# Performance work log

Measured on AMD Instinct MI355X. Metric: run time of the kernel, lower is better.

The kernel has to match this reference:

```python
import jax, jax.numpy as jnp
import numpy as np

H = 48; W = 48; WS = 8; NH = 12; FTH = 0.4; EPS = 1e-6


def _layernorm(x, w, b):
    mu = jnp.mean(x, axis=-1, keepdims=True)
    var = jnp.mean((x - mu) ** 2, axis=-1, keepdims=True)
    return (x - mu) * jax.lax.rsqrt(var + EPS) * w + b


def _mha(x, w_qkv, b_qkv, w_o, b_o, key_mask=None):
    # x: (Bn, N, C); w_qkv: (3, C, C); key_mask: (Bn, N) bool or None
    Bn, N, C = x.shape
    d = C // NH
    qkv = jnp.einsum('bnc,tcd->tbnd', x, w_qkv) + b_qkv[:, None, None, :]
    q, k, v = [t.reshape(Bn, N, NH, d).transpose(0, 2, 1, 3) for t in qkv]
    s = jnp.einsum('bhqd,bhkd->bhqk', q, k) / jnp.sqrt(jnp.asarray(d, x.dtype))
    if key_mask is not None:
        s = jnp.where(key_mask[:, None, None, :], s, jnp.asarray(-1e9, s.dtype))
    p = jax.nn.softmax(s, axis=-1)
    ctx = jnp.einsum('bhqk,bhkd->bhqd', p, v).transpose(0, 2, 1, 3).reshape(Bn, N, C)
    return ctx @ w_o + b_o


def _forward(x, mask, w_qkv_g, b_qkv_g, w_o_g, b_o_g, w_qkv_l, b_qkv_l, w_o_l, b_o_l,
             ln1_w, ln1_b, ln2_w, ln2_b, w_fc1, b_fc1, w_fc2, b_fc2):
    B, L, C = x.shape
    shortcut = x
    xn = _layernorm(x, ln1_w, ln1_b)

    # avg_pool2d(mask, 4, 4) -> (B, H, W); fg/bg split
    pooled = mask.reshape(B, 1, H, 4, W, 4).mean(axis=(3, 5))[:, 0]      # (B,H,W)
    fg = pooled > FTH                                                    # bool (B,H,W)
    fg_tok = fg.reshape(B, L)
    bg = (~fg).astype(x.dtype)
    # window-level bg mask: avg_pool(bg, WS) > 0 -> window contains any bg token
    bg_win = bg.reshape(B, H // WS, WS, W // WS, WS).mean(axis=(2, 4)) > 0.0   # (B, nH, nW)
    bg_win_tok = jnp.broadcast_to(bg_win[:, :, None, :, None],
                                  (B, H // WS, WS, W // WS, WS)).reshape(B, L)

    # local windowed attention on all windows (equivalent on bg windows; masked out elsewhere)
    xw = xn.reshape(B, H // WS, WS, W // WS, WS, C).transpose(0, 1, 3, 2, 4, 5)
    xw = xw.reshape(-1, WS * WS, C)                                      # (B*nWin, WS*WS, C)
    lout = _mha(xw, w_qkv_l, b_qkv_l, w_o_l, b_o_l)
    lout = lout.reshape(B, H // WS, W // WS, WS, WS, C).transpose(0, 1, 3, 2, 4, 5)
    lout = lout.reshape(B, L, C)

    # global attention with fg key mask (fg queries attend fg keys only)
    gout = _mha(xn, w_qkv_g, b_qkv_g, w_o_g, b_o_g, key_mask=fg_tok)

    # scatter-back semantics: fg positions take global output; bg-window positions take local output; rest zero
    zero = jnp.zeros((), x.dtype)
    x_new = jnp.where(fg_tok[..., None], gout,
                      jnp.where(bg_win_tok[..., None], lout, zero))

    x1 = shortcut + x_new
    h = _layernorm(x1, ln2_w, ln2_b)
    h = jax.nn.gelu(h @ w_fc1 + b_fc1, approximate=False) @ w_fc2 + b_fc2
    return x1 + h


def setup_inputs() -> dict:
    key = jax.random.key(0)
    ks = jax.random.split(key, 8)
    B, L, C, M = 2, H * W, 768, 3072
    s = 0.02
    return {
        'x': jax.random.normal(ks[0], (B, L, C), jnp.float32),
        'mask': jax.random.uniform(ks[1], (B, 1, 4 * H, 4 * W), jnp.float32),
        'w_qkv_g': jax.random.normal(ks[2], (3, C, C), jnp.float32) * s,
        'b_qkv_g': jnp.zeros((3, C), jnp.float32),
        'w_o_g': jax.random.normal(ks[3], (C, C), jnp.float32) * s,
        'b_o_g': jnp.zeros((C,), jnp.float32),
        'w_qkv_l': jax.random.normal(ks[4], (3, C, C), jnp.float32) * s,
        'b_qkv_l': jnp.zeros((3, C), jnp.float32),
        'w_o_l': jax.random.normal(ks[5], (C, C), jnp.float32) * s,
        'b_o_l': jnp.zeros((C,), jnp.float32),
        'ln1_w': jnp.ones((C,), jnp.float32),
        'ln1_b': jnp.zeros((C,), jnp.float32),
        'ln2_w': jnp.ones((C,), jnp.float32),
        'ln2_b': jnp.zeros((C,), jnp.float32),
        'w_fc1': jax.random.normal(ks[6], (C, M), jnp.float32) * s,
        'b_fc1': jnp.zeros((M,), jnp.float32),
        'w_fc2': jax.random.normal(ks[7], (M, C), jnp.float32) * s,
        'b_fc2': jnp.zeros((C,), jnp.float32),
    }


def reference(x, mask, w_qkv_g, b_qkv_g, w_o_g, b_o_g, w_qkv_l, b_qkv_l, w_o_l, b_o_l,
              ln1_w, ln1_b, ln2_w, ln2_b, w_fc1, b_fc1, w_fc2, b_fc2):
    return _forward(x, mask, w_qkv_g, b_qkv_g, w_o_g, b_o_g, w_qkv_l, b_qkv_l, w_o_l, b_o_l,
                    ln1_w, ln1_b, ln2_w, ln2_b, w_fc1, b_fc1, w_fc2, b_fc2)
```

## Files before the change

### kernel.cpp

```cpp
#include <hip/hip_runtime.h>
#include <math.h>

#define Lh 2304
#define Ch 768
#define NHh 12
#define Bh 2
#define QS2 3072

typedef unsigned short ushort_t;
typedef unsigned int uint_t;
typedef __attribute__((ext_vector_type(8))) short bf16x8;
typedef __attribute__((ext_vector_type(4))) float f32x4;
#define MFMA16(a, b, c) __builtin_amdgcn_mfma_f32_16x16x32_bf16(a, b, c, 0, 0, 0)

#define SCL2 0.18033688f
#define MSK2 1.4426950e9f
#if __has_builtin(__builtin_amdgcn_exp2f)
#define EXP2F(x) __builtin_amdgcn_exp2f(x)
#else
#define EXP2F(x) exp2f(x)
#endif

__device__ __forceinline__ ushort_t f2bf(float f) {
    union { float f; uint_t u; } v; v.f = f;
    uint_t u = v.u + 0x7fffu + ((v.u >> 16) & 1u);
    return (ushort_t)(u >> 16);
}
__device__ __forceinline__ uint_t pack2bf(float a, float b) {
    return (uint_t)f2bf(a) | ((uint_t)f2bf(b) << 16);
}

__device__ __forceinline__ void llds16(ushort_t* dst, const ushort_t* src) {
    __builtin_amdgcn_global_load_lds(
        (__attribute__((address_space(1))) void*)(const_cast<ushort_t*>(src)),
        (__attribute__((address_space(3))) void*)dst, 16, 0, 0);
}

__global__ __launch_bounds__(256)
void layernorm_bf16_kernel(const float* __restrict__ x, const float* __restrict__ w,
                           const float* __restrict__ b, ushort_t* __restrict__ y)
{
    int row = blockIdx.x;
    int tid = threadIdx.x;
    const float* xr = x + (size_t)row * Ch;
    float v0 = xr[tid], v1 = xr[tid + 256], v2 = xr[tid + 512];
    __shared__ float red[256];
    red[tid] = v0 + v1 + v2;
    __syncthreads();
    for (int st = 128; st > 0; st >>= 1) {
        if (tid < st) red[tid] += red[tid + st];
        __syncthreads();
    }
    float mean = red[0] * (1.0f / 768.0f);
    __syncthreads();
    float d0 = v0 - mean, d1 = v1 - mean, d2 = v2 - mean;
    red[tid] = d0 * d0 + d1 * d1 + d2 * d2;
    __syncthreads();
    for (int st = 128; st > 0; st >>= 1) {
        if (tid < st) red[tid] += red[tid + st];
        __syncthreads();
    }
    float rstd = rsqrtf(red[0] * (1.0f / 768.0f) + 1e-6f);
    ushort_t* yr = y + (size_t)row * Ch;
    yr[tid]       = f2bf(d0 * rstd * w[tid]       + b[tid]);
    yr[tid + 256] = f2bf(d1 * rstd * w[tid + 256] + b[tid + 256]);
    yr[tid + 512] = f2bf(d2 * rstd * w[tid + 512] + b[tid + 512]);
}

__global__ __launch_bounds__(64)
void mask_kernel(const float* __restrict__ mask, float* __restrict__ fg,
                 float* __restrict__ bgw)
{
    int win = blockIdx.x;
    int b = win / 36, w = win % 36;
    int wi = w / 6, wj = w % 6;
    int lane = threadIdx.x;
    int i = wi * 8 + (lane >> 3), j = wj * 8 + (lane & 7);
    const float* mb = mask + (size_t)b * 192 * 192 + (size_t)(i * 4) * 192 + j * 4;
    float s = 0.0f;
    #pragma unroll
    for (int di = 0; di < 4; ++di) {
        float4 v = *(const float4*)(mb + (size_t)di * 192);
        s += v.x + v.y + v.z + v.w;
    }
    float f = (s * (1.0f / 16.0f) > 0.4f) ? 1.0f : 0.0f;
    fg[b * Lh + i * 48 + j] = f;
    unsigned long long bg = __ballot(f == 0.0f);
    if (lane == 0) bgw[win] = bg ? 1.0f : 0.0f;
}

__global__ __launch_bounds__(256)
void transpose_all_kernel(const float* __restrict__ w_qkv_g, const float* __restrict__ w_qkv_l,
                          const float* __restrict__ w_o_g, const float* __restrict__ w_o_l,
                          const float* __restrict__ w_fc1, const float* __restrict__ w_fc2,
                          ushort_t* __restrict__ wtq, ushort_t* __restrict__ wt_o_g,
                          ushort_t* __restrict__ wt_o_l, ushort_t* __restrict__ wt_fc1,
                          ushort_t* __restrict__ wt_fc2)
{
    int blk = blockIdx.x;
    const float* W; ushort_t* D; int K, N, nx, bx;
    const size_t CC = (size_t)Ch * Ch;
    if (blk < 432)       { int t = blk / 144; bx = blk % 144;
                           W = w_qkv_g + t * CC; D = wtq + t * CC; K = 768; N = 768; nx = 12; }
    else if (blk < 864)  { int r = blk - 432; int t = r / 144; bx = r % 144;
                           W = w_qkv_l + t * CC; D = wtq + (size_t)2304 * 768 + t * CC;
                           K = 768; N = 768; nx = 12; }
    else if (blk < 1008) { bx = blk - 864;  W = w_o_g; D = wt_o_g; K = 768; N = 768; nx = 12; }
    else if (blk < 1152) { bx = blk - 1008; W = w_o_l; D = wt_o_l; K = 768; N = 768; nx = 12; }
    else if (blk < 1728) { bx = blk - 1152; W = w_fc1; D = wt_fc1; K = 768; N = 3072; nx = 48; }
    else                 { bx = blk - 1728; W = w_fc2; D = wt_fc2; K = 3072; N = 768; nx = 12; }
    int n0 = (bx % nx) * 64;
    int k0 = (bx / nx) * 64;
    int tid = threadIdx.x;
    __shared__ float T[64][65];
    #pragma unroll
    for (int i = 0; i < 16; ++i) {
        int lin = i * 256 + tid;
        int r = lin >> 6, c = lin & 63;
        T[r][c] = W[(size_t)(k0 + r) * N + n0 + c];
    }
    __syncthreads();
    #pragma unroll
    for (int i = 0; i < 4; ++i) {
        int lin = i * 256 + tid;
        int r = lin >> 4, c0 = (lin & 15) * 4;
        uint_t lo = pack2bf(T[c0][r], T[c0 + 1][r]);
        uint_t hi = pack2bf(T[c0 + 2][r], T[c0 + 3][r]);
        *(uint2*)&D[(size_t)(n0 + r) * K + k0 + c0] = make_uint2(lo, hi);
    }
}

template<int BNt, int VMODE>
__global__ __launch_bounds__(256)
void gemm_bf16_t(const ushort_t* __restrict__ A, const ushort_t* __restrict__ Bt,
                 const float* __restrict__ bias, const float* __restrict__ residual,
                 void* __restrict__ C, ushort_t* __restrict__ vt,
                 int M, int N, int K, int flags)
{
    __shared__ ushort_t AsL[2][128 * 32];
    __shared__ ushort_t BsL[2][BNt * 32];
    int bm = blockIdx.y * 128;
    int bx = blockIdx.x;
    int bn;
    if (VMODE == 1) {
        bn = (bx < 6) ? 1536 + bx * 128 : 3840 + (bx - 6) * 128;
    } else if (flags & 4) {
        bn = (bx < 12) ? bx * 128 : 2304 + (bx - 12) * 128;
    } else {
        bn = bx * BNt;
    }
    int tid = threadIdx.x;
    int lane = tid & 63;
    int wave = tid >> 6;
    int wm = wave >> 1, wn = wave & 1;
    int quad = lane >> 4, l15 = lane & 15;
    constexpr int NJ = BNt / 32;

    int srow = lane >> 2;
    int sg8 = ((lane & 3) ^ ((lane >> 3) & 3)) * 8;
    int fsw = (l15 >> 1) & 3;

    f32x4 acc[4][NJ];
    #pragma unroll
    for (int i = 0; i < 4; ++i)
        #pragma unroll
        for (int j = 0; j < NJ; ++j)
            acc[i][j] = (f32x4){0.f, 0.f, 0.f, 0.f};

    int iters = K / 32;
    llds16(&AsL[0][wave * 512], A + (size_t)(bm + wave * 16 + srow) * K + sg8);
    llds16(&AsL[0][(wave + 4) * 512], A + (size_t)(bm + (wave + 4) * 16 + srow) * K + sg8);
    llds16(&BsL[0][wave * 512], Bt + (size_t)(bn + wave * 16 + srow) * K + sg8);
    if (BNt == 128)
        llds16(&BsL[0][(wave + 4) * 512], Bt + (size_t)(bn + (wave + 4) * 16 + srow) * K + sg8);

    for (int kt = 0; kt < iters; ++kt) {
        int cur = kt & 1;
        __syncthreads();

        bf16x8 af[4], bfr[NJ];
        #pragma unroll
        for (int i = 0; i < 4; ++i)
            af[i] = *(const bf16x8*)&AsL[cur][(wm * 64 + i * 16 + l15) * 32 + ((quad ^ fsw) * 8)];
        #pragma unroll
        for (int j = 0; j < NJ; ++j)
            bfr[j] = *(const bf16x8*)&BsL[cur][(wn * (BNt / 2) + j * 16 + l15) * 32 + ((quad ^ fsw) * 8)];

        if (kt + 1 < iters) {
            int k0 = (kt + 1) * 32;
            int nxt = 1 - cur;
            llds16(&AsL[nxt][wave * 512], A + (size_t)(bm + wave * 16 + srow) * K + k0 + sg8);
            llds16(&AsL[nxt][(wave + 4) * 512], A + (size_t)(bm + (wave + 4) * 16 + srow) * K + k0 + sg8);
            llds16(&BsL[nxt][wave * 512], Bt + (size_t)(bn + wave * 16 + srow) * K + k0 + sg8);
            if (BNt == 128)
                llds16(&BsL[nxt][(wave + 4) * 512], Bt + (size_t)(bn + (wave + 4) * 16 + srow) * K + k0 + sg8);
        }

        if constexpr (VMODE == 0) {
            #pragma unroll
            for (int i = 0; i < 4; ++i)
                #pragma unroll
                for (int j = 0; j < NJ; ++j)
                    acc[i][j] = MFMA16(bfr[j], af[i], acc[i][j]);
        } else {
            #pragma unroll
            for (int i = 0; i < 4; ++i)
                #pragma unroll
                for (int j = 0; j < NJ; ++j)
                    acc[i][j] = MFMA16(af[i], bfr[j], acc[i][j]);
        }
    }

    if constexpr (VMODE == 1) {
        #pragma unroll
        for (int j = 0; j < NJ; ++j) {
            int col = bn + wn * (BNt / 2) + j * 16 + l15;
            int colp = col - ((col >= 3840) ? 3072 : 1536);
            float bc = bias[col];
            #pragma unroll
            for (int i = 0; i < 4; ++i) {
                int row0 = bm + wm * 64 + i * 16 + quad * 4;
                *(uint2*)&vt[(size_t)colp * 4608 + row0] =
                    make_uint2(pack2bf(acc[i][j][0] + bc, acc[i][j][1] + bc),
                               pack2bf(acc[i][j][2] + bc, acc[i][j][3] + bc));
            }
        }
        return;
    }

    #pragma unroll
    for (int i = 0; i < 4; ++i) {
        int row = bm + wm * 64 + i * 16 + l15;
        #pragma unroll
        for (int j = 0; j < NJ; ++j) {
            int col = bn + wn * (BNt / 2) + j * 16 + quad * 4;
            float4 bia = *(const float4*)&bias[col];
            float o0 = acc[i][j][0] + bia.x;
            float o1 = acc[i][j][1] + bia.y;
            float o2 = acc[i][j][2] + bia.z;
            float o3 = acc[i][j][3] + bia.w;
            if (flags & 1) {
                o0 = o0 * 0.5f * (1.0f + erff(o0 * 0.70710678f));
                o1 = o1 * 0.5f * (1.0f + erff(o1 * 0.70710678f));
                o2 = o2 * 0.5f * (1.0f + erff(o2 * 0.70710678f));
                o3 = o3 * 0.5f * (1.0f + erff(o3 * 0.70710678f));
            }
            if (residual) {
                float4 rs = *(const float4*)&residual[(size_t)row * N + col];
                o0 += rs.x; o1 += rs.y; o2 += rs.z; o3 += rs.w;
            }
            if (flags & 4) {
                int cq = col - ((col >= 2304) ? 768 : 0);
                *(uint2*)&((ushort_t*)C)[(size_t)row * QS2 + cq] =
                    make_uint2(pack2bf(o0, o1), pack2bf(o2, o3));
            } else if (flags & 2) {
                *(uint2*)&((ushort_t*)C)[(size_t)row * N + col] =
                    make_uint2(pack2bf(o0, o1), pack2bf(o2, o3));
            } else {
                *(float4*)&((float*)C)[(size_t)row * N + col] =
                    make_float4(o0, o1, o2, o3);
            }
        }
    }
}

__global__ __launch_bounds__(256)
void oproj_dual_kernel(const ushort_t* __restrict__ ctxg, const ushort_t* __restrict__ ctxl,
                       const ushort_t* __restrict__ Wg, const ushort_t* __restrict__ Wl,
                       const float* __restrict__ biasg, const float* __restrict__ biasl,
                       const float* __restrict__ x, float* __restrict__ x1,
                       const float* __restrict__ fg, const float* __restrict__ bgw)
{
    __shared__ ushort_t AsL[2][128 * 32];
    __shared__ ushort_t BsL[2][64 * 32];
    int bm = blockIdx.y * 128;
    int bn = blockIdx.x * 64;
    int tid = threadIdx.x;
    int lane = tid & 63;
    int wave = tid >> 6;
    int wm = wave >> 1, wn = wave & 1;
    int quad = lane >> 4, l15 = lane & 15;

    int srow = lane >> 2;
    int sg8 = ((lane & 3) ^ ((lane >> 3) & 3)) * 8;
    int fsw = (l15 >> 1) & 3;
    const int K = Ch, N = Ch, iters = Ch / 32;

    f32x4 accg[4][2], accl[4][2];
    #pragma unroll
    for (int i = 0; i < 4; ++i)
        #pragma unroll
        for (int j = 0; j < 2; ++j) {
            accg[i][j] = (f32x4){0.f, 0.f, 0.f, 0.f};
            accl[i][j] = (f32x4){0.f, 0.f, 0.f, 0.f};
        }

    #pragma unroll
    for (int pass = 0; pass < 2; ++pass) {
        const ushort_t* A = pass ? ctxl : ctxg;
        const ushort_t* Bt = pass ? Wl : Wg;
        if (pass) __syncthreads();
        llds16(&AsL[0][wave * 512], A + (size_t)(bm + wave * 16 + srow) * K + sg8);
        llds16(&AsL[0][(wave + 4) * 512], A + (size_t)(bm + (wave + 4) * 16 + srow) * K + sg8);
        llds16(&BsL[0][wave * 512], Bt + (size_t)(bn + wave * 16 + srow) * K + sg8);

        for (int kt = 0; kt < iters; ++kt) {
            int cur = kt & 1;
            __syncthreads();
            bf16x8 af[4], bfr[2];
            #pragma unroll
            for (int i = 0; i < 4; ++i)
                af[i] = *(const bf16x8*)&AsL[cur][(wm * 64 + i * 16 + l15) * 32 + ((quad ^ fsw) * 8)];
            #pragma unroll
            for (int j = 0; j < 2; ++j)
                bfr[j] = *(const bf16x8*)&BsL[cur][(wn * 32 + j * 16 + l15) * 32 + ((quad ^ fsw) * 8)];
            if (kt + 1 < iters) {
                int k0 = (kt + 1) * 32;
                int nxt = 1 - cur;
                llds16(&AsL[nxt][wave * 512], A + (size_t)(bm + wave * 16 + srow) * K + k0 + sg8);
                llds16(&AsL[nxt][(wave + 4) * 512], A + (size_t)(bm + (wave + 4) * 16 + srow) * K + k0 + sg8);
                llds16(&BsL[nxt][wave * 512], Bt + (size_t)(bn + wave * 16 + srow) * K + k0 + sg8);
            }
            if (pass == 0) {
                #pragma unroll
                for (int i = 0; i < 4; ++i)
                    #pragma unroll
                    for (int j = 0; j < 2; ++j)
                        accg[i][j] = MFMA16(bfr[j], af[i], accg[i][j]);
            } else {
                #pragma unroll
                for (int i = 0; i < 4; ++i)
                    #pragma unroll
                    for (int j = 0; j < 2; ++j)
                        accl[i][j] = MFMA16(bfr[j], af[i], accl[i][j]);
            }
        }
    }

    #pragma unroll
    for (int i = 0; i < 4; ++i) {
        int row = bm + wm * 64 + i * 16 + l15;
        int bb = (row >= Lh) ? 1 : 0;
        int n = row - bb * Lh;
        int ii = n / 48, jj = n % 48;
        float keepg = (fg[row] != 0.0f) ? 1.0f : 0.0f;
        float keepl = (keepg == 0.0f &&
                       bgw[bb * 36 + (ii >> 3) * 6 + (jj >> 3)] != 0.0f) ? 1.0f : 0.0f;
        #pragma unroll
        for (int j = 0; j < 2; ++j) {
            int col = bn + wn * 32 + j * 16 + quad * 4;
            float4 bg4 = *(const float4*)&biasg[col];
            float4 bl4 = *(const float4*)&biasl[col];
            float4 x4 = *(const float4*)&x[(size_t)row * N + col];
            float4 o;
            o.x = x4.x + keepg * (accg[i][j][0] + bg4.x) + keepl * (accl[i][j][0] + bl4.x);
            o.y = x4.y + keepg * (accg[i][j][1] + bg4.y) + keepl * (accl[i][j][1] + bl4.y);
            o.z = x4.z + keepg * (accg[i][j][2] + bg4.z) + keepl * (accl[i][j][2] + bl4.z);
            o.w = x4.w + keepg * (accg[i][j][3] + bg4.w) + keepl * (accl[i][j][3] + bl4.w);
            *(float4*)&x1[(size_t)row * N + col] = o;
        }
    }
}

__device__ __forceinline__ void attn_global_body(
    const ushort_t* __restrict__ QKV, const ushort_t* __restrict__ VT,
    const float* __restrict__ fg,
    float* __restrict__ Opart, float* __restrict__ Lpart,
    int tile, int h, int b, int half,
    ushort_t (*Ks)[2][64][32], ushort_t (*Vs)[2][64][32],
    ushort_t (*Ps)[72], float (*fgs)[64])
{
    int tid = threadIdx.x;
    int lane = tid & 63;
    int wave = tid >> 6;
    int quad = lane >> 4, l15 = lane & 15;
    int kb0 = half * 1152;

    bf16x8 aq[2][2];
    #pragma unroll
    for (int s = 0; s < 2; ++s) {
        int tok = tile * 128 + wave * 32 + s * 16 + l15;
        const ushort_t* qbase = QKV + (size_t)(b * Lh + tok) * QS2 + h * 64;
        #pragma unroll
        for (int step = 0; step < 2; ++step)
            aq[s][step] = *(const bf16x8*)(qbase + step * 32 + quad * 8);
    }

    int srow = lane >> 2;
    int sc = lane & 3;
    int krow = wave * 16 + srow;
    int scx = (sc ^ ((krow >> 1) & 3)) * 8;
    const ushort_t* ksrc = QKV + (size_t)(b * Lh + kb0 + krow) * QS2 + 768 + h * 64 + scx;
    const ushort_t* vsrc = VT + (size_t)(h * 64 + krow) * 4608 + b * Lh + kb0 + scx;

    float l_part[2] = {0.f, 0.f};
    f32x4 o_acc[2][4];
    #pragma unroll
    for (int s = 0; s < 2; ++s)
        #pragma unroll
        for (int t4 = 0; t4 < 4; ++t4) o_acc[s][t4] = (f32x4){0.f, 0.f, 0.f, 0.f};

    llds16(&Ks[0][0][wave * 16][0], ksrc);
    llds16(&Ks[0][1][wave * 16][0], ksrc + 32);
    llds16(&Vs[0][0][wave * 16][0], vsrc);
    llds16(&Vs[0][1][wave * 16][0], vsrc + 32);
    if (tid < 64) fgs[0][tid] = (fg[b * Lh + kb0 + tid] - 1.0f) * MSK2;

    int rfs = (l15 >> 1) & 3;

    for (int kt = 0; kt < 18; ++kt) {
        int cur = kt & 1, nxt = cur ^ 1;
        __syncthreads();

        bf16x8 bk[2][4];
        #pragma unroll
        for (int step = 0; step < 2; ++step)
            #pragma unroll
            for (int j4 = 0; j4 < 4; ++j4)
                bk[step][j4] = *(const bf16x8*)&Ks[cur][step][j4 * 16 + l15][(quad ^ rfs) * 8];

        if (kt + 1 < 18) {
            const ushort_t* kp = ksrc + (size_t)(kt + 1) * 64 * QS2;
            const ushort_t* vp = vsrc + (kt + 1) * 64;
            llds16(&Ks[nxt][0][wave * 16][0], kp);
            llds16(&Ks[nxt][1][wave * 16][0], kp + 32);
            llds16(&Vs[nxt][0][wave * 16][0], vp);
            llds16(&Vs[nxt][1][wave * 16][0], vp + 32);
            if (tid < 64) fgs[nxt][tid] = (fg[b * Lh + kb0 + (kt + 1) * 64 + tid] - 1.0f) * MSK2;
        }

        f32x4 s4[2][4];
        #pragma unroll
        for (int s = 0; s < 2; ++s)
            #pragma unroll
            for (int j4 = 0; j4 < 4; ++j4) s4[s][j4] = (f32x4){0.f, 0.f, 0.f, 0.f};
        #pragma unroll
        for (int step = 0; step < 2; ++step)
            #pragma unroll
            for (int s = 0; s < 2; ++s)
                #pragma unroll
                for (int j4 = 0; j4 < 4; ++j4)
                    s4[s][j4] = MFMA16(bk[step][j4], aq[s][step], s4[s][j4]);

        #pragma unroll
        for (int s = 0; s < 2; ++s) {
            int p0 = wave * 32 + s * 16;
            #pragma unroll
            for (int j4 = 0; j4 < 4; ++j4) {
                float4 mb4 = *(const float4*)&fgs[cur][j4 * 16 + quad * 4];
                float e0 = EXP2F(s4[s][j4][0] * SCL2 + mb4.x);
                float e1 = EXP2F(s4[s][j4][1] * SCL2 + mb4.y);
                float e2 = EXP2F(s4[s][j4][2] * SCL2 + mb4.z);
                float e3 = EXP2F(s4[s][j4][3] * SCL2 + mb4.w);
                l_part[s] += (e0 + e1) + (e2 + e3);
                uint_t a01 = __builtin_amdgcn_perm(__float_as_uint(e1), __float_as_uint(e0), 0x07060302u);
                uint_t a23 = __builtin_amdgcn_perm(__float_as_uint(e3), __float_as_uint(e2), 0x07060302u);
                *(uint2*)&Ps[p0 + l15][j4 * 16 + quad * 4] = make_uint2(a01, a23);
            }
        }
        #pragma unroll
        for (int step = 0; step < 2; ++step) {
            bf16x8 bv[4];
            #pragma unroll
            for (int t4 = 0; t4 < 4; ++t4)
                bv[t4] = *(const bf16x8*)&Vs[cur][step][t4 * 16 + l15][(quad ^ rfs) * 8];
            #pragma unroll
            for (int s = 0; s < 2; ++s) {
                int p0 = wave * 32 + s * 16;
                bf16x8 a = *(const bf16x8*)&Ps[p0 + l15][step * 32 + quad * 8];
                #pragma unroll
                for (int t4 = 0; t4 < 4; ++t4)
                    o_acc[s][t4] = MFMA16(bv[t4], a, o_acc[s][t4]);
            }
        }
    }

    #pragma unroll
    for (int s = 0; s < 2; ++s) {
        float v = l_part[s];
        v += __shfl_xor(v, 16, 64);
        v += __shfl_xor(v, 32, 64);
        int ql = wave * 32 + s * 16 + l15;
        int tok = tile * 128 + ql;
        float* op = Opart + ((size_t)half * 4608 + b * Lh + tok) * Ch + h * 64;
        #pragma unroll
        for (int t4 = 0; t4 < 4; ++t4)
            *(f32x4*)&op[t4 * 16 + quad * 4] = o_acc[s][t4];
        if (quad == 0)
            Lpart[((size_t)half * 4608 + b * Lh + tok) * NHh + h] = v;
    }
}

__device__ __forceinline__ void attn_local_body(
    const ushort_t* __restrict__ QKV, const ushort_t* __restrict__ VT,
    ushort_t* __restrict__ O, int tile, int h, int b,
    ushort_t (*Ks)[2][64][32], ushort_t (*Vs)[2][64][32], ushort_t (*Ps)[72])
{
    int tid = threadIdx.x;
    int lane = tid & 63;
    int wave = tid >> 6;
    int quad = lane >> 4, l15 = lane & 15;
    int wi = tile / 6, wj = tile % 6;

    bf16x8 aq[2];
    {
        int ql = wave * 16 + l15;
        int tok = (wi * 8 + (ql >> 3)) * 48 + wj * 8 + (ql & 7);
        const ushort_t* qbase = QKV + (size_t)(b * Lh + tok) * QS2 + 1536 + h * 64;
        #pragma unroll
        for (int step = 0; step < 2; ++step)
            aq[step] = *(const bf16x8*)(qbase + step * 32 + quad * 8);
    }

    {
        int srow = lane >> 2;
        int sc = lane & 3;
        int krow = wave * 16 + srow;
        int kfs = (krow >> 1) & 3;
        int tokK = (wi * 8 + (krow >> 3)) * 48 + wj * 8 + (krow & 7);
        const ushort_t* ksrc = QKV + (size_t)(b * Lh + tokK) * QS2 + 2304 + h * 64 + (sc ^ kfs) * 8;
        int c0 = sc ^ kfs;
        const ushort_t* vbase = VT + (size_t)(768 + h * 64 + krow) * 4608 + b * Lh + wj * 8;
        llds16(&Ks[0][0][wave * 16][0], ksrc);
        llds16(&Ks[0][1][wave * 16][0], ksrc + 32);
        llds16(&Vs[0][0][wave * 16][0], vbase + (wi * 8 + c0) * 48);
        llds16(&Vs[0][1][wave * 16][0], vbase + (wi * 8 + 4 + c0) * 48);
    }
    __syncthreads();

    float l_part = 0.f;
    f32x4 o_acc[4];
    #pragma unroll
    for (int t4 = 0; t4 < 4; ++t4) o_acc[t4] = (f32x4){0.f, 0.f, 0.f, 0.f};

    int rfs = (l15 >> 1) & 3;
    f32x4 s4[4];
    #pragma unroll
    for (int j4 = 0; j4 < 4; ++j4) s4[j4] = (f32x4){0.f, 0.f, 0.f, 0.f};
    #pragma unroll
    for (int step = 0; step < 2; ++step) {
        bf16x8 bk[4];
        #pragma unroll
        for (int j4 = 0; j4 < 4; ++j4)
            bk[j4] = *(const bf16x8*)&Ks[0][step][j4 * 16 + l15][(quad ^ rfs) * 8];
        #pragma unroll
        for (int j4 = 0; j4 < 4; ++j4)
            s4[j4] = MFMA16(bk[j4], aq[step], s4[j4]);
    }
    int p0 = wave * 16;
    #pragma unroll
    for (int j4 = 0; j4 < 4; ++j4) {
        float e0 = EXP2F(s4[j4][0] * SCL2);
        float e1 = EXP2F(s4[j4][1] * SCL2);
        float e2 = EXP2F(s4[j4][2] * SCL2);
        float e3 = EXP2F(s4[j4][3] * SCL2);
        l_part += (e0 + e1) + (e2 + e3);
        uint_t a01 = __builtin_amdgcn_perm(__float_as_uint(e1), __float_as_uint(e0), 0x07060302u);
        uint_t a23 = __builtin_amdgcn_perm(__float_as_uint(e3), __float_as_uint(e2), 0x07060302u);
        *(uint2*)&Ps[p0 + l15][j4 * 16 + quad * 4] = make_uint2(a01, a23);
    }
    #pragma unroll
    for (int step = 0; step < 2; ++step) {
        bf16x8 bv[4];
        #pragma unroll
        for (int t4 = 0; t4 < 4; ++t4)
            bv[t4] = *(const bf16x8*)&Vs[0][step][t4 * 16 + l15][(quad ^ rfs) * 8];
        bf16x8 a = *(const bf16x8*)&Ps[p0 + l15][step * 32 + quad * 8];
        #pragma unroll
        for (int t4 = 0; t4 < 4; ++t4)
            o_acc[t4] = MFMA16(bv[t4], a, o_acc[t4]);
    }

    {
        float v = l_part;
        v += __shfl_xor(v, 16, 64);
        v += __shfl_xor(v, 32, 64);
        float inv = 1.0f / v;
        int ql = wave * 16 + l15;
        int tok = (wi * 8 + (ql >> 3)) * 48 + wj * 8 + (ql & 7);
        ushort_t* ob = O + (size_t)(b * Lh + tok) * Ch + h * 64;
        #pragma unroll
        for (int t4 = 0; t4 < 4; ++t4) {
            *(uint2*)&ob[t4 * 16 + quad * 4] =
                make_uint2(pack2bf(o_acc[t4][0] * inv, o_acc[t4][1] * inv),
                           pack2bf(o_acc[t4][2] * inv, o_acc[t4][3] * inv));
        }
    }
}

__global__ __launch_bounds__(256)
void attn_fused_kernel(const ushort_t* __restrict__ QKV, const ushort_t* __restrict__ VT,
                       const float* __restrict__ fg,
                       float* __restrict__ Opart, float* __restrict__ Lpart,
                       ushort_t* __restrict__ ctxl)
{
    __shared__ __align__(16) ushort_t Ks[2][2][64][32];
    __shared__ __align__(16) ushort_t Vs[2][2][64][32];
    __shared__ __align__(16) ushort_t Ps[128][72];
    __shared__ float fgs[2][64];

    int bid = blockIdx.x;
    if (bid < 864) {
        int gid = (bid & 7) * 108 + (bid >> 3);
        int half = gid / 432;
        int rem = gid % 432;
        int tile = rem % 18;
        int h = (rem / 18) % NHh;
        int b = rem / 216;
        attn_global_body(QKV, VT, fg, Opart, Lpart, tile, h, b, half, Ks, Vs, Ps, fgs);
    } else {
        int rr = bid - 864;
        int lid = (rr & 7) * 108 + (rr >> 3);
        int tile = lid % 36;
        int h = (lid / 36) % NHh;
        int b = lid / 432;
        attn_local_body(QKV, VT, ctxl, tile, h, b, Ks, Vs, Ps);
    }
}

__global__ __launch_bounds__(192)
void attn_merge_kernel(const float* __restrict__ Op, const float* __restrict__ Lp,
                       ushort_t* __restrict__ ctxg)
{
    int r = blockIdx.x;
    int tid = threadIdx.x;
    int d = tid * 4;
    int h = d >> 6;
    float la = Lp[(size_t)r * NHh + h];
    float lb = Lp[((size_t)4608 + r) * NHh + h];
    float inv = 1.0f / (la + lb);
    const float* pa = Op + (size_t)r * Ch + d;
    const float* pb = Op + (size_t)4608 * Ch + (size_t)r * Ch + d;
    float4 a = *(const float4*)pa;
    float4 b4 = *(const float4*)pb;
    *(uint2*)&ctxg[(size_t)r * Ch + d] =
        make_uint2(pack2bf((a.x + b4.x) * inv, (a.y + b4.y) * inv),
                   pack2bf((a.z + b4.z) * inv, (a.w + b4.w) * inv));
}

extern "C" void kernel_launch(void* const* d_in, const int* in_sizes, int n_in,
                              void* d_out, int out_size, void* d_ws, size_t ws_size,
                              hipStream_t stream)
{
    const float* x       = (const float*)d_in[0];
    const float* mask    = (const float*)d_in[1];
    const float* w_qkv_g = (const float*)d_in[2];
    const float* b_qkv_g = (const float*)d_in[3];
    const float* w_o_g   = (const float*)d_in[4];
    const float* b_o_g   = (const float*)d_in[5];
    const float* w_qkv_l = (const float*)d_in[6];
    const float* b_qkv_l = (const float*)d_in[7];
    const float* w_o_l   = (const float*)d_in[8];
    const float* b_o_l   = (const float*)d_in[9];
    const float* ln1_w   = (const float*)d_in[10];
    const float* ln1_b   = (const float*)d_in[11];
    const float* ln2_w   = (const float*)d_in[12];
    const float* ln2_b   = (const float*)d_in[13];
    const float* w_fc1   = (const float*)d_in[14];
    const float* b_fc1   = (const float*)d_in[15];
    const float* w_fc2   = (const float*)d_in[16];
    const float* b_fc2   = (const float*)d_in[17];
    float* out = (float*)d_out;

    const size_t U = (size_t)Bh * Lh * Ch;
    char* p = (char*)d_ws;
    ushort_t* qkvb = (ushort_t*)p;        p += (size_t)4608 * 3072 * 2;
    ushort_t* vtb  = (ushort_t*)p;        p += (size_t)1536 * 4608 * 2;
    ushort_t* midb = qkvb;
    ushort_t* ctxg = (ushort_t*)p;        p += U * 2;
    ushort_t* ctxl = (ushort_t*)p;        p += U * 2;
    ushort_t* xnb  = (ushort_t*)p;        p += U * 2;
    float*    Opart = (float*)p;          p += (size_t)2 * U * 4;
    float*    Lpart = (float*)p;          p += (size_t)2 * 4608 * NHh * 4;
    float*    x1   = Opart;
    ushort_t* wtq  = (ushort_t*)p;        p += (size_t)4608 * 768 * 2;
    ushort_t* wt_o_g = (ushort_t*)p;      p += (size_t)768 * 768 * 2;
    ushort_t* wt_o_l = (ushort_t*)p;      p += (size_t)768 * 768 * 2;
    ushort_t* wt_fc1 = (ushort_t*)p;      p += (size_t)3072 * 768 * 2;
    ushort_t* wt_fc2 = (ushort_t*)p;      p += (size_t)768 * 3072 * 2;
    float*    biasq  = (float*)p;         p += 4608 * 4;
    float*    fg     = (float*)p;         p += Bh * Lh * 4;
    float*    bgw    = (float*)p;

    const int Mrows = Bh * Lh;
    dim3 blk(256);

    hipMemcpyAsync(biasq, b_qkv_g, 2304 * sizeof(float), hipMemcpyDeviceToDevice, stream);
    hipMemcpyAsync(biasq + 2304, b_qkv_l, 2304 * sizeof(float), hipMemcpyDeviceToDevice, stream);

    transpose_all_kernel<<<2304, blk, 0, stream>>>(
        w_qkv_g, w_qkv_l, w_o_g, w_o_l, w_fc1, w_fc2,
        wtq, wt_o_g, wt_o_l, wt_fc1, wt_fc2);

    layernorm_bf16_kernel<<<Mrows, blk, 0, stream>>>(x, ln1_w, ln1_b, xnb);
    mask_kernel<<<72, dim3(64), 0, stream>>>(mask, fg, bgw);

    gemm_bf16_t<128, 0><<<dim3(24, Mrows / 128), blk, 0, stream>>>(
        xnb, wtq, biasq, nullptr, qkvb, nullptr, Mrows, 4608, Ch, 4);
    gemm_bf16_t<128, 1><<<dim3(12, Mrows / 128), blk, 0, stream>>>(
        xnb, wtq, biasq, nullptr, nullptr, vtb, Mrows, 4608, Ch, 4);

    attn_fused_kernel<<<1728, blk, 0, stream>>>(qkvb, vtb, fg, Opart, Lpart, ctxl);
    attn_merge_kernel<<<Mrows, dim3(192), 0, stream>>>(Opart, Lpart, ctxg);

    oproj_dual_kernel<<<dim3(Ch / 64, Mrows / 128), blk, 0, stream>>>(
        ctxg, ctxl, wt_o_g, wt_o_l, b_o_g, b_o_l, x, x1, fg, bgw);

    layernorm_bf16_kernel<<<Mrows, blk, 0, stream>>>(x1, ln2_w, ln2_b, xnb);

    gemm_bf16_t<128, 0><<<dim3(3072 / 128, Mrows / 128), blk, 0, stream>>>(
        xnb, wt_fc1, b_fc1, nullptr, midb, nullptr, Mrows, 3072, Ch, 1 | 2);
    gemm_bf16_t<64, 0><<<dim3(Ch / 64, Mrows / 128), blk, 0, stream>>>(
        midb, wt_fc2, b_fc2, x1, out, nullptr, Mrows, Ch, 3072, 0);
}
```

Baseline: 406.4 us.

## Fuse launches, single-pass dual o-proj, and raise MFMA priority in attention

Two hipMemcpyAsync calls for the QKV bias are folded into extra blocks of the weight transpose kernel, and the mask pooling is merged into the first layernorm launch, which removes several small launches. The dual output-projection kernel now streams the global and local operands together in one K loop with separate LDS buffers, replacing two sequential passes. The attention kernel wraps its MFMA sections in s_setprio to favour matrix issue. The o-proj change doubles LDS use per block, which may lower occupancy.

New measurement: 404.0 us. No clear change (-0.6%).

```diff
diff --git a/kernel.cpp b/kernel.cpp
--- a/kernel.cpp
+++ b/kernel.cpp
@@ -36,15 +36,13 @@
         (__attribute__((address_space(3))) void*)dst, 16, 0, 0);
 }
 
-__global__ __launch_bounds__(256)
-void layernorm_bf16_kernel(const float* __restrict__ x, const float* __restrict__ w,
-                           const float* __restrict__ b, ushort_t* __restrict__ y)
-{
-    int row = blockIdx.x;
+__device__ __forceinline__ void ln_body(const float* __restrict__ x, const float* __restrict__ w,
+                                        const float* __restrict__ b, ushort_t* __restrict__ y,
+                                        int row, float* red)
+{
     int tid = threadIdx.x;
     const float* xr = x + (size_t)row * Ch;
     float v0 = xr[tid], v1 = xr[tid + 256], v2 = xr[tid + 512];
-    __shared__ float red[256];
     red[tid] = v0 + v1 + v2;
     __syncthreads();
     for (int st = 128; st > 0; st >>= 1) {
@@ -67,16 +65,33 @@
     yr[tid + 512] = f2bf(d2 * rstd * w[tid + 512] + b[tid + 512]);
 }
 
-__global__ __launch_bounds__(64)
-void mask_kernel(const float* __restrict__ mask, float* __restrict__ fg,
-                 float* __restrict__ bgw)
-{
-    int win = blockIdx.x;
-    int b = win / 36, w = win % 36;
-    int wi = w / 6, wj = w % 6;
-    int lane = threadIdx.x;
-    int i = wi * 8 + (lane >> 3), j = wj * 8 + (lane & 7);
-    const float* mb = mask + (size_t)b * 192 * 192 + (size_t)(i * 4) * 192 + j * 4;
+__global__ __launch_bounds__(256)
+void layernorm_bf16_kernel(const float* __restrict__ x, const float* __restrict__ w,
+                           const float* __restrict__ b, ushort_t* __restrict__ y)
+{
+    __shared__ float red[256];
+    ln_body(x, w, b, y, blockIdx.x, red);
+}
+
+__global__ __launch_bounds__(256)
+void ln_mask_kernel(const float* __restrict__ x, const float* __restrict__ w,
+                    const float* __restrict__ b, ushort_t* __restrict__ y,
+                    const float* __restrict__ mask, float* __restrict__ fg,
+                    float* __restrict__ bgw)
+{
+    __shared__ float red[256];
+    int bid = blockIdx.x;
+    if (bid < 4608) {
+        ln_body(x, w, b, y, bid, red);
+        return;
+    }
+    int win = bid - 4608;
+    int tid = threadIdx.x;
+    if (tid >= 64) return;
+    int bb = win / 36, ww = win % 36;
+    int wi = ww / 6, wj = ww % 6;
+    int i = wi * 8 + (tid >> 3), j = wj * 8 + (tid & 7);
+    const float* mb = mask + (size_t)bb * 192 * 192 + (size_t)(i * 4) * 192 + j * 4;
     float s = 0.0f;
     #pragma unroll
     for (int di = 0; di < 4; ++di) {
@@ -84,20 +99,29 @@
         s += v.x + v.y + v.z + v.w;
     }
     float f = (s * (1.0f / 16.0f) > 0.4f) ? 1.0f : 0.0f;
-    fg[b * Lh + i * 48 + j] = f;
+    fg[bb * Lh + i * 48 + j] = f;
     unsigned long long bg = __ballot(f == 0.0f);
-    if (lane == 0) bgw[win] = bg ? 1.0f : 0.0f;
+    if (tid == 0) bgw[win] = bg ? 1.0f : 0.0f;
 }
 
 __global__ __launch_bounds__(256)
 void transpose_all_kernel(const float* __restrict__ w_qkv_g, const float* __restrict__ w_qkv_l,
                           const float* __restrict__ w_o_g, const float* __restrict__ w_o_l,
                           const float* __restrict__ w_fc1, const float* __restrict__ w_fc2,
+                          const float* __restrict__ b_qkv_g, const float* __restrict__ b_qkv_l,
                           ushort_t* __restrict__ wtq, ushort_t* __restrict__ wt_o_g,
                           ushort_t* __restrict__ wt_o_l, ushort_t* __restrict__ wt_fc1,
-                          ushort_t* __restrict__ wt_fc2)
+                          ushort_t* __restrict__ wt_fc2, float* __restrict__ biasq)
 {
     int blk = blockIdx.x;
+    int tid = threadIdx.x;
+    if (blk >= 2304) {
+        int which = blk - 2304;
+        const float* src = which ? b_qkv_l : b_qkv_g;
+        float* dst = biasq + which * 2304;
+        for (int i = tid; i < 2304; i += 256) dst[i] = src[i];
+        return;
+    }
     const float* W; ushort_t* D; int K, N, nx, bx;
     const size_t CC = (size_t)Ch * Ch;
     if (blk < 432)       { int t = blk / 144; bx = blk % 144;
@@ -111,7 +135,6 @@
     else                 { bx = blk - 1728; W = w_fc2; D = wt_fc2; K = 3072; N = 768; nx = 12; }
     int n0 = (bx % nx) * 64;
     int k0 = (bx / nx) * 64;
-    int tid = threadIdx.x;
     __shared__ float T[64][65];
     #pragma unroll
     for (int i = 0; i < 16; ++i) {
@@ -271,8 +294,10 @@
                        const float* __restrict__ x, float* __restrict__ x1,
                        const float* __restrict__ fg, const float* __restrict__ bgw)
 {
-    __shared__ ushort_t AsL[2][128 * 32];
-    __shared__ ushort_t BsL[2][64 * 32];
+    __shared__ ushort_t AgL[2][128 * 32];
+    __shared__ ushort_t AlL[2][128 * 32];
+    __shared__ ushort_t BgL[2][64 * 32];
+    __shared__ ushort_t BlL[2][64 * 32];
     int bm = blockIdx.y * 128;
     int bn = blockIdx.x * 64;
     int tid = threadIdx.x;
@@ -295,46 +320,47 @@
             accl[i][j] = (f32x4){0.f, 0.f, 0.f, 0.f};
         }
 
-    #pragma unroll
-    for (int pass = 0; pass < 2; ++pass) {
-        const ushort_t* A = pass ? ctxl : ctxg;
-        const ushort_t* Bt = pass ? Wl : Wg;
-        if (pass) __syncthreads();
-        llds16(&AsL[0][wave * 512], A + (size_t)(bm + wave * 16 + srow) * K + sg8);
-        llds16(&AsL[0][(wave + 4) * 512], A + (size_t)(bm + (wave + 4) * 16 + srow) * K + sg8);
-        llds16(&BsL[0][wave * 512], Bt + (size_t)(bn + wave * 16 + srow) * K + sg8);
-
-        for (int kt = 0; kt < iters; ++kt) {
-            int cur = kt & 1;
-            __syncthreads();
-            bf16x8 af[4], bfr[2];
-            #pragma unroll
-            for (int i = 0; i < 4; ++i)
-                af[i] = *(const bf16x8*)&AsL[cur][(wm * 64 + i * 16 + l15) * 32 + ((quad ^ fsw) * 8)];
+    llds16(&AgL[0][wave * 512], ctxg + (size_t)(bm + wave * 16 + srow) * K + sg8);
+    llds16(&AgL[0][(wave + 4) * 512], ctxg + (size_t)(bm + (wave + 4) * 16 + srow) * K + sg8);
+    llds16(&AlL[0][wave * 512], ctxl + (size_t)(bm + wave * 16 + srow) * K + sg8);
+    llds16(&AlL[0][(wave + 4) * 512], ctxl + (size_t)(bm + (wave + 4) * 16 + srow) * K + sg8);
+    llds16(&BgL[0][wave * 512], Wg + (size_t)(bn + wave * 16 + srow) * K + sg8);
+    llds16(&BlL[0][wave * 512], Wl + (size_t)(bn + wave * 16 + srow) * K + sg8);
+
+    for (int kt = 0; kt < iters; ++kt) {
+        int cur = kt & 1;
+        __syncthreads();
+        bf16x8 afg[4], afl[4], bfg[2], bfl[2];
+        #pragma unroll
+        for (int i = 0; i < 4; ++i) {
+            afg[i] = *(const bf16x8*)&AgL[cur][(wm * 64 + i * 16 + l15) * 32 + ((quad ^ fsw) * 8)];
+            afl[i] = *(const bf16x8*)&AlL[cur][(wm * 64 + i * 16 + l15) * 32 + ((quad ^ fsw) * 8)];
+        }
+        #pragma unroll
+        for (int j = 0; j < 2; ++j) {
+            bfg[j] = *(const bf16x8*)&BgL[cur][(wn * 32 + j * 16 + l15) * 32 + ((quad ^ fsw) * 8)];
+            bfl[j] = *(const bf16x8*)&BlL[cur][(wn * 32 + j * 16 + l15) * 32 + ((quad ^ fsw) * 8)];
+        }
+        if (kt + 1 < iters) {
+            int k0 = (kt + 1) * 32;
+            int nxt = 1 - cur;
+            llds16(&AgL[nxt][wave * 512], ctxg + (size_t)(bm + wave * 16 + srow) * K + k0 + sg8);
+            llds16(&AgL[nxt][(wave + 4) * 512], ctxg + (size_t)(bm + (wave + 4) * 16 + srow) * K + k0 + sg8);
+            llds16(&AlL[nxt][wave * 512], ctxl + (size_t)(bm + wave * 16 + srow) * K + k0 + sg8);
+            llds16(&AlL[nxt][(wave + 4) * 512], ctxl + (size_t)(bm + (wave + 4) * 16 + srow) * K + k0 + sg8);
+            llds16(&BgL[nxt][wave * 512], Wg + (size_t)(bn + wave * 16 + srow) * K + k0 + sg8);
+            llds16(&BlL[nxt][wave * 512], Wl + (size_t)(bn + wave * 16 + srow) * K + k0 + sg8);
+        }
+        #pragma unroll
+        for (int i = 0; i < 4; ++i)
             #pragma unroll
             for (int j = 0; j < 2; ++j)
-                bfr[j] = *(const bf16x8*)&BsL[cur][(wn * 32 + j * 16 + l15) * 32 + ((quad ^ fsw) * 8)];
-            if (kt + 1 < iters) {
-                int k0 = (kt + 1) * 32;
-                int nxt = 1 - cur;
-                llds16(&AsL[nxt][wave * 512], A + (size_t)(bm + wave * 16 + srow) * K + k0 + sg8);
-                llds16(&AsL[nxt][(wave + 4) * 512], A + (size_t)(bm + (wave + 4) * 16 + srow) * K + k0 + sg8);
-                llds16(&BsL[nxt][wave * 512], Bt + (size_t)(bn + wave * 16 + srow) * K + k0 + sg8);
-            }
-            if (pass == 0) {
-                #pragma unroll
-                for (int i = 0; i < 4; ++i)
-                    #pragma unroll
-                    for (int j = 0; j < 2; ++j)
-                        accg[i][j] = MFMA16(bfr[j], af[i], accg[i][j]);
-            } else {
-                #pragma unroll
-                for (int i = 0; i < 4; ++i)
-                    #pragma unroll
-                    for (int j = 0; j < 2; ++j)
-                        accl[i][j] = MFMA16(bfr[j], af[i], accl[i][j]);
-            }
-        }
+                accg[i][j] = MFMA16(bfg[j], afg[i], accg[i][j]);
+        #pragma unroll
+        for (int i = 0; i < 4; ++i)
+            #pragma unroll
+            for (int j = 0; j < 2; ++j)
+                accl[i][j] = MFMA16(bfl[j], afl[i], accl[i][j]);
     }
 
     #pragma unroll
@@ -434,6 +460,7 @@
         for (int s = 0; s < 2; ++s)
             #pragma unroll
             for (int j4 = 0; j4 < 4; ++j4) s4[s][j4] = (f32x4){0.f, 0.f, 0.f, 0.f};
+        __builtin_amdgcn_s_setprio(1);
         #pragma unroll
         for (int step = 0; step < 2; ++step)
             #pragma unroll
@@ -441,6 +468,7 @@
                 #pragma unroll
                 for (int j4 = 0; j4 < 4; ++j4)
                     s4[s][j4] = MFMA16(bk[step][j4], aq[s][step], s4[s][j4]);
+        __builtin_amdgcn_s_setprio(0);
 
         #pragma unroll
         for (int s = 0; s < 2; ++s) {
@@ -464,6 +492,7 @@
             #pragma unroll
             for (int t4 = 0; t4 < 4; ++t4)
                 bv[t4] = *(const bf16x8*)&Vs[cur][step][t4 * 16 + l15][(quad ^ rfs) * 8];
+            __builtin_amdgcn_s_setprio(1);
             #pragma unroll
             for (int s = 0; s < 2; ++s) {
                 int p0 = wave * 32 + s * 16;
@@ -472,6 +501,7 @@
                 for (int t4 = 0; t4 < 4; ++t4)
                     o_acc[s][t4] = MFMA16(bv[t4], a, o_acc[s][t4]);
             }
+            __builtin_amdgcn_s_setprio(0);
         }
     }
 
@@ -685,15 +715,11 @@
     const int Mrows = Bh * Lh;
     dim3 blk(256);
 
-    hipMemcpyAsync(biasq, b_qkv_g, 2304 * sizeof(float), hipMemcpyDeviceToDevice, stream);
-    hipMemcpyAsync(biasq + 2304, b_qkv_l, 2304 * sizeof(float), hipMemcpyDeviceToDevice, stream);
-
-    transpose_all_kernel<<<2304, blk, 0, stream>>>(
-        w_qkv_g, w_qkv_l, w_o_g, w_o_l, w_fc1, w_fc2,
-        wtq, wt_o_g, wt_o_l, wt_fc1, wt_fc2);
-
-    layernorm_bf16_kernel<<<Mrows, blk, 0, stream>>>(x, ln1_w, ln1_b, xnb);
-    mask_kernel<<<72, dim3(64), 0, stream>>>(mask, fg, bgw);
+    transpose_all_kernel<<<2306, blk, 0, stream>>>(
+        w_qkv_g, w_qkv_l, w_o_g, w_o_l, w_fc1, w_fc2, b_qkv_g, b_qkv_l,
+        wtq, wt_o_g, wt_o_l, wt_fc1, wt_fc2, biasq);
+
+    ln_mask_kernel<<<4680, blk, 0, stream>>>(x, ln1_w, ln1_b, xnb, mask, fg, bgw);
 
     gemm_bf16_t<128, 0><<<dim3(24, Mrows / 128), blk, 0, stream>>>(
         xnb, wtq, biasq, nullptr, qkvb, nullptr, Mrows, 4608, Ch, 4);
```
